# Kernel optimization log

Measured on AMD Instinct MI355X. Metric: run time of the kernel, lower is better.

The kernel has to match this reference:

```python
import jax, jax.numpy as jnp
import numpy as np

NT = 128          # num_timesteps (reference query points)
E = 128           # embed_time
H = 128           # nhidden
NH = 1            # num_heads
F = 32            # feature_size
NS = 2            # num_states
EPS = 1e-5


def layer_norm(x, g, b):
    m = jnp.mean(x, axis=-1, keepdims=True)
    v = jnp.mean((x - m) ** 2, axis=-1, keepdims=True)
    return (x - m) * jax.lax.rsqrt(v + EPS) * g + b


def setup_inputs() -> dict:
    key = jax.random.key(0)
    ks = jax.random.split(key, 24)
    nrm = lambda k, s: (jax.random.normal(k, s) * 0.05).astype(jnp.float32)
    inp = {
        "input": jax.random.normal(ks[0], (8, F, 512), dtype=jnp.float32),
        "mask": jax.random.randint(ks[1], (8, F, 512), 0, 2).astype(jnp.float32),
        "timesteps": jnp.sort(jax.random.uniform(ks[2], (8, 512), dtype=jnp.float32), axis=-1),
        # time embedding
        "periodic_w": nrm(ks[3], (E - 1, 1)), "periodic_b": nrm(ks[4], (E - 1,)),
        "lin_w": nrm(ks[5], (1, 1)), "lin_b": nrm(ks[6], (1,)),
        # query / key projections + layer norms
        "q_w": nrm(ks[7], (E, E)), "q_b": nrm(ks[8], (E,)),
        "q_g": jnp.ones((E,), jnp.float32), "q_be": jnp.zeros((E,), jnp.float32),
        "k_w": nrm(ks[9], (E, E)), "k_b": nrm(ks[10], (E,)),
        "k_g": jnp.ones((E,), jnp.float32), "k_be": jnp.zeros((E,), jnp.float32),
        # attention_norm over h*2F channels, then output linear + LN to nhidden
        "attn_g": jnp.ones((NH * 2 * F,), jnp.float32), "attn_b": jnp.zeros((NH * 2 * F,), jnp.float32),
        "out_w": nrm(ks[11], (H, NH * 2 * F)), "out_b": nrm(ks[12], (H,)),
        "out_g": jnp.ones((H,), jnp.float32), "out_be": jnp.zeros((H,), jnp.float32),
        # GRU (torch gate order r, z, n)
        "gru_wih": nrm(ks[13], (3 * H, H)), "gru_whh": nrm(ks[14], (3 * H, H)),
        "gru_bih": nrm(ks[15], (3 * H,)), "gru_bhh": nrm(ks[16], (3 * H,)),
        # classifier MLP
        "c1_w": nrm(ks[17], (H, H)), "c1_b": nrm(ks[18], (H,)),
        "c2_w": nrm(ks[19], (H, H)), "c2_b": nrm(ks[20], (H,)),
        "c3_w": nrm(ks[21], (NS, H)), "c3_b": nrm(ks[22], (NS,)),
    }
    return inp


def time_embedding(tt, lin_w, lin_b, periodic_w, periodic_b):
    t = tt[..., None]                                   # (..., 1)
    out1 = t @ lin_w.T + lin_b                          # (..., 1)
    out2 = jnp.sin(t @ periodic_w.T + periodic_b)       # (..., E-1)
    return jnp.concatenate([out1, out2], axis=-1)       # (..., E)


def reference(input, mask, timesteps, periodic_w, periodic_b, lin_w, lin_b,
              q_w, q_b, q_g, q_be, k_w, k_b, k_g, k_be,
              attn_g, attn_b, out_w, out_b, out_g, out_be,
              gru_wih, gru_whh, gru_bih, gru_bhh,
              c1_w, c1_b, c2_w, c2_b, c3_w, c3_b):
    B = input.shape[0]
    x_in = jnp.transpose(input, (0, 2, 1))              # (B, T, F)
    m = 1.0 - jnp.transpose(mask, (0, 2, 1))            # (B, T, F)
    x_in = x_in * (m > 0).astype(x_in.dtype)
    x = jnp.concatenate([x_in, m], axis=-1)             # (B, T, 2F)
    mk = jnp.concatenate([m, m], axis=-1)               # (B, T, 2F)

    key_e = time_embedding(timesteps, lin_w, lin_b, periodic_w, periodic_b)        # (B, T, E)
    qtimes = jnp.linspace(0.0, 1.0, NT)
    query_e = time_embedding(qtimes[None], lin_w, lin_b, periodic_w, periodic_b)   # (1, NT, E)

    q = layer_norm(query_e @ q_w.T + q_b, q_g, q_be)    # (1, NT, E)
    k = layer_norm(key_e @ k_w.T + k_b, k_g, k_be)      # (B, T, E)

    etk = E // NH
    q = q.reshape(1, NT, NH, etk).transpose(0, 2, 1, 3)         # (1, h, NT, etk)
    k = k.reshape(B, -1, NH, etk).transpose(0, 2, 1, 3)         # (B, h, T, etk)

    scores = jnp.einsum("ahqd,bhkd->bhqk", q, k) / np.sqrt(etk)  # (B, h, NT, T)
    # per-channel masked softmax over keys: (B, h, NT, T, 2F)
    logits = jnp.where(mk[:, None, None, :, :] == 0, -1e9, scores[..., None])
    p_attn = jax.nn.softmax(logits, axis=-2)
    att = jnp.sum(p_attn * x[:, None, None, :, :], axis=-2)     # (B, h, NT, 2F)

    x2 = att.transpose(0, 2, 1, 3).reshape(B, NT, NH * 2 * F)
    x2 = layer_norm(x2, attn_g, attn_b)
    out = layer_norm(x2 @ out_w.T + out_b, out_g, out_be)       # (B, NT, H)

    # GRU over the NT reference timesteps, last hidden state
    seq = out.transpose(1, 0, 2)                                # (NT, B, H)
    h0 = jnp.zeros((B, H), out.dtype)

    def gru_step(h, x_t):
        gi = x_t @ gru_wih.T + gru_bih
        gh = h @ gru_whh.T + gru_bhh
        ir, iz, inn = jnp.split(gi, 3, axis=-1)
        hr, hz, hn = jnp.split(gh, 3, axis=-1)
        r = jax.nn.sigmoid(ir + hr)
        z = jax.nn.sigmoid(iz + hz)
        n = jnp.tanh(inn + r * hn)
        h_new = (1.0 - z) * n + z * h
        return h_new, None

    h_last, _ = jax.lax.scan(gru_step, h0, seq)

    h1 = jax.nn.relu(h_last @ c1_w.T + c1_b)
    h2 = jax.nn.relu(h1 @ c2_w.T + c2_b)
    return h2 @ c3_w.T + c3_b                                   # (B, num_states) logits
```

## Files before the change

### kernel.cpp

```cpp
#include <hip/hip_runtime.h>
#include <math.h>

#define LN_EPS 1e-5f

typedef _Float16 h2v __attribute__((ext_vector_type(2)));

__device__ __forceinline__ float dot4(float4 a, float4 b) {
    return a.x*b.x + a.y*b.y + a.z*b.z + a.w*b.w;
}
__device__ __forceinline__ void fma4(float4& a, float s, float4 v) {
    a.x += s*v.x; a.y += s*v.y; a.z += s*v.z; a.w += s*v.w;
}
__device__ __forceinline__ float fast_rcp(float x) {
    return __builtin_amdgcn_rcpf(x);
}
__device__ __forceinline__ float fast_sigmoid(float x) {
    return fast_rcp(1.f + __expf(-x));
}
__device__ __forceinline__ float fast_tanh(float x) {
    return 1.f - 2.f*fast_rcp(__expf(2.f*x) + 1.f);
}
__device__ __forceinline__ float fdot2u(unsigned int a, unsigned int b, float c) {
#if __has_builtin(__builtin_amdgcn_fdot2)
    return __builtin_amdgcn_fdot2(__builtin_bit_cast(h2v, a),
                                  __builtin_bit_cast(h2v, b), c, false);
#else
    const h2v av = __builtin_bit_cast(h2v, a);
    const h2v bv = __builtin_bit_cast(h2v, b);
    return c + (float)av[0]*(float)bv[0] + (float)av[1]*(float)bv[1];
#endif
}
__device__ __forceinline__ float wsum64(float v) {
    #pragma unroll
    for (int off = 32; off > 0; off >>= 1) v += __shfl_xor(v, off);
    return v;
}

__global__ void k_embed_proj(
    const float* __restrict__ input, const float* __restrict__ mask,
    const float* __restrict__ timesteps,
    const float* __restrict__ pw, const float* __restrict__ pb,
    const float* __restrict__ lw, const float* __restrict__ lb,
    const float* __restrict__ q_w, const float* __restrict__ q_b,
    const float* __restrict__ q_g, const float* __restrict__ q_be,
    const float* __restrict__ k_w, const float* __restrict__ k_b,
    const float* __restrict__ k_g, const float* __restrict__ k_be,
    float* __restrict__ qs, float* __restrict__ kT, float2* __restrict__ xm)
{
    const int blk = blockIdx.x;
    const int tid = threadIdx.x;

    __shared__ __align__(16) float e[4][128];
    __shared__ __align__(16) float4 red[128];
    __shared__ __align__(16) float proj[4][128];
    __shared__ __align__(16) float2 tile[32][65];

    if (blk < 64) {
        const int b  = blk >> 3;
        const int t0 = (blk & 7) * 64;
        const int cg = tid >> 6;
        const int tt = tid & 63;
        #pragma unroll
        for (int c16 = 0; c16 < 16; ++c16) {
            const int c = c16*2 + cg;
            const float m = mask [(size_t)(b*32 + c)*512 + t0 + tt];
            const float x = input[(size_t)(b*32 + c)*512 + t0 + tt];
            const float mm = 1.0f - m;
            tile[c][tt] = make_float2(x*mm, mm);
        }
        __syncthreads();
        const int c2 = tid & 31;
        const int tg = tid >> 5;
        #pragma unroll
        for (int k = 0; k < 16; ++k) {
            const int t = tg*16 + k;
            xm[((size_t)b*512 + t0 + t)*32 + c2] = tile[c2][t];
        }
        return;
    }

    const bool isq = blk < 96;
    float tv[4];
    int kidx0 = 0;
    if (isq) {
        const int q0 = (blk - 64) * 4;
        #pragma unroll
        for (int r = 0; r < 4; ++r) tv[r] = (float)(q0 + r) * (1.0f/127.0f);
    } else {
        kidx0 = (blk - 96) * 4;
        #pragma unroll
        for (int r = 0; r < 4; ++r) tv[r] = timesteps[kidx0 + r];
    }

    float pwj = 0.f, pbj = 0.f;
    if (tid > 0) { pwj = pw[tid-1]; pbj = pb[tid-1]; }
    const float lw0 = lw[0], lb0 = lb[0];
    #pragma unroll
    for (int r = 0; r < 4; ++r)
        e[r][tid] = (tid == 0) ? (tv[r]*lw0 + lb0) : sinf(tv[r]*pwj + pbj);
    __syncthreads();

    const float* W  = isq ? q_w  : k_w;
    const float* Bv = isq ? q_b  : k_b;
    const float* G  = isq ? q_g  : k_g;
    const float* Be = isq ? q_be : k_be;

    {
        const int jj = tid >> 2, dc = tid & 3;
        const float4* e0 = (const float4*)(&e[0][0]);
        const float4* e1 = (const float4*)(&e[1][0]);
        const float4* e2 = (const float4*)(&e[2][0]);
        const float4* e3 = (const float4*)(&e[3][0]);
        #pragma unroll
        for (int jb = 0; jb < 4; ++jb) {
            const int j = jb*32 + jj;
            const float4* wrow = (const float4*)(W + (size_t)j*128);
            float a0=0.f, a1=0.f, a2=0.f, a3=0.f;
            #pragma unroll
            for (int k = 0; k < 8; ++k) {
                const int idx = dc + 4*k;
                const float4 w4 = wrow[idx];
                a0 += dot4(w4, e0[idx]);
                a1 += dot4(w4, e1[idx]);
                a2 += dot4(w4, e2[idx]);
                a3 += dot4(w4, e3[idx]);
            }
            a0 += __shfl_xor(a0, 1, 4); a0 += __shfl_xor(a0, 2, 4);
            a1 += __shfl_xor(a1, 1, 4); a1 += __shfl_xor(a1, 2, 4);
            a2 += __shfl_xor(a2, 1, 4); a2 += __shfl_xor(a2, 2, 4);
            a3 += __shfl_xor(a3, 1, 4); a3 += __shfl_xor(a3, 2, 4);
            if (dc == 0) {
                const float bj = Bv[j];
                proj[0][j] = a0 + bj; proj[1][j] = a1 + bj;
                proj[2][j] = a2 + bj; proj[3][j] = a3 + bj;
            }
        }
    }
    __syncthreads();

    float acc[4];
    #pragma unroll
    for (int r = 0; r < 4; ++r) acc[r] = proj[r][tid];

    red[tid] = make_float4(acc[0], acc[1], acc[2], acc[3]);
    __syncthreads();
    for (int s = 64; s > 0; s >>= 1) {
        if (tid < s) {
            float4 m = red[tid]; const float4 o = red[tid+s];
            m.x += o.x; m.y += o.y; m.z += o.z; m.w += o.w;
            red[tid] = m;
        }
        __syncthreads();
    }
    float4 mean = red[0];
    mean.x *= (1.0f/128.0f); mean.y *= (1.0f/128.0f);
    mean.z *= (1.0f/128.0f); mean.w *= (1.0f/128.0f);
    __syncthreads();
    const float d0 = acc[0]-mean.x, d1 = acc[1]-mean.y,
                d2 = acc[2]-mean.z, d3 = acc[3]-mean.w;
    red[tid] = make_float4(d0*d0, d1*d1, d2*d2, d3*d3);
    __syncthreads();
    for (int s = 64; s > 0; s >>= 1) {
        if (tid < s) {
            float4 m = red[tid]; const float4 o = red[tid+s];
            m.x += o.x; m.y += o.y; m.z += o.z; m.w += o.w;
            red[tid] = m;
        }
        __syncthreads();
    }
    float4 var = red[0];
    var.x *= (1.0f/128.0f); var.y *= (1.0f/128.0f);
    var.z *= (1.0f/128.0f); var.w *= (1.0f/128.0f);

    const float gg = G[tid], bb = Be[tid];
    const float o0 = d0*rsqrtf(var.x+LN_EPS)*gg + bb;
    const float o1 = d1*rsqrtf(var.y+LN_EPS)*gg + bb;
    const float o2 = d2*rsqrtf(var.z+LN_EPS)*gg + bb;
    const float o3 = d3*rsqrtf(var.w+LN_EPS)*gg + bb;

    if (isq) {
        const float sc = 0.08838834764831845f;
        const int q0 = (blk - 64)*4;
        qs[(size_t)(q0+0)*128 + tid] = o0*sc;
        qs[(size_t)(q0+1)*128 + tid] = o1*sc;
        qs[(size_t)(q0+2)*128 + tid] = o2*sc;
        qs[(size_t)(q0+3)*128 + tid] = o3*sc;
    } else {
        const int b = kidx0 >> 9;
        const int t = kidx0 & 511;
        *(float4*)(kT + ((size_t)(b*128 + tid))*512 + t) =
            make_float4(o0, o1, o2, o3);
    }
}

__global__ void __launch_bounds__(256) k_attn(
    const float2* __restrict__ xm,
    const float* __restrict__ qs, const float* __restrict__ kT,
    const float* __restrict__ attn_g, const float* __restrict__ attn_b,
    const float* __restrict__ out_w, const float* __restrict__ out_b,
    const float* __restrict__ out_g, const float* __restrict__ out_be,
    float* __restrict__ outm)
{
    const int b     = blockIdx.x >> 5;
    const int qbase = (blockIdx.x & 31) * 4;
    const int tid   = threadIdx.x;

    __shared__ __align__(16) float et[4][512];
    __shared__ __align__(16) float qsh[4][128];
    __shared__ __align__(16) float wsh[128*66];
    __shared__ __align__(16) float sA[4][8][32];
    __shared__ __align__(16) float aA[4][8][32];
    __shared__ __align__(16) float x2s[4][64];
    __shared__ float redC[4];

    for (int idx = tid; idx < 512; idx += 256)
        qsh[idx >> 7][idx & 127] = qs[(size_t)(qbase + (idx >> 7))*128 + (idx & 127)];
    for (int idx = tid; idx < 8192; idx += 256)
        wsh[(idx >> 6)*66 + (idx & 63)] = out_w[idx];
    __syncthreads();

    {
        const int grp = tid >> 7;
        const int tl  = tid & 127;
        const int q0  = grp*2;
        const float4* kp  = (const float4*)kT + (size_t)b*128*128 + tl;
        const float4* qa4 = (const float4*)qsh[q0];
        const float4* qb4 = (const float4*)qsh[q0+1];
        float4 a0 = make_float4(0,0,0,0), a1 = make_float4(0,0,0,0);
        float4 c0 = kp[0], c1 = kp[128], c2 = kp[256], c3 = kp[384];
        for (int c = 0; c < 32; ++c) {
            float4 n0, n1, n2, n3;
            if (c < 31) {
                const float4* kn = kp + (size_t)(4*c+4)*128;
                n0 = kn[0]; n1 = kn[128]; n2 = kn[256]; n3 = kn[384];
            }
            const float4 qa = qa4[c], qb = qb4[c];
            fma4(a0, qa.x, c0); fma4(a1, qb.x, c0);
            fma4(a0, qa.y, c1); fma4(a1, qb.y, c1);
            fma4(a0, qa.z, c2); fma4(a1, qb.z, c2);
            fma4(a0, qa.w, c3); fma4(a1, qb.w, c3);
            c0 = n0; c1 = n1; c2 = n2; c3 = n3;
        }
        a0.x = __expf(a0.x); a0.y = __expf(a0.y); a0.z = __expf(a0.z); a0.w = __expf(a0.w);
        a1.x = __expf(a1.x); a1.y = __expf(a1.y); a1.z = __expf(a1.z); a1.w = __expf(a1.w);
        ((float4*)et[q0])[tl]   = a0;
        ((float4*)et[q0+1])[tl] = a1;
    }
    __syncthreads();

    {
        const int c   = tid & 31;
        const int seg = tid >> 5;
        const float2* xp = xm + ((size_t)b*512 + seg*64)*32 + c;
        float s0=0,s1=0,s2=0,s3=0, a0=0,a1=0,a2=0,a3=0;
        #pragma unroll 4
        for (int i = 0; i < 64; ++i) {
            const float2 v = xp[(size_t)i*32];
            const int t = seg*64 + i;
            const float w0 = et[0][t]*v.y, w1 = et[1][t]*v.y;
            const float w2 = et[2][t]*v.y, w3 = et[3][t]*v.y;
            s0 += w0; s1 += w1; s2 += w2; s3 += w3;
            a0 += w0*v.x; a1 += w1*v.x; a2 += w2*v.x; a3 += w3*v.x;
        }
        sA[0][seg][c]=s0; sA[1][seg][c]=s1; sA[2][seg][c]=s2; sA[3][seg][c]=s3;
        aA[0][seg][c]=a0; aA[1][seg][c]=a1; aA[2][seg][c]=a2; aA[3][seg][c]=a3;
    }
    __syncthreads();

    {
        const int ql = tid >> 6;
        const int c2 = tid & 63;
        const int cc = c2 & 31;
        float ss = 0.f;
        #pragma unroll
        for (int g = 0; g < 8; ++g) ss += sA[ql][g][cc];
        float attv;
        if (c2 < 32) {
            float aa = 0.f;
            #pragma unroll
            for (int g = 0; g < 8; ++g) aa += aA[ql][g][cc];
            attv = (ss > 0.f) ? aa/ss : 0.f;
        } else {
            attv = (ss > 0.f) ? 1.0f : 0.0f;
        }
        const float mean = wsum64(attv) * (1.0f/64.0f);
        const float dv = attv - mean;
        const float var = wsum64(dv*dv) * (1.0f/64.0f);
        x2s[ql][c2] = dv*rsqrtf(var+LN_EPS)*attn_g[c2] + attn_b[c2];
    }
    __syncthreads();

    {
        const int jhalf = tid >> 7;
        const int j     = tid & 127;
        const int wave  = tid >> 6;
        for (int lq2 = 0; lq2 < 2; ++lq2) {
            const int ql = jhalf*2 + lq2;
            float acc = out_b[j];
            const float4* wrow = (const float4*)(wsh + j*66);
            const float4* xr   = (const float4*)x2s[ql];
            #pragma unroll
            for (int k = 0; k < 16; ++k) acc += dot4(wrow[k], xr[k]);

            float v = wsum64(acc);
            if ((tid & 63) == 0) redC[wave] = v;
            __syncthreads();
            const float mean = (redC[jhalf*2] + redC[jhalf*2+1]) * (1.0f/128.0f);
            __syncthreads();
            const float d = acc - mean;
            v = wsum64(d*d);
            if ((tid & 63) == 0) redC[wave] = v;
            __syncthreads();
            const float var = (redC[jhalf*2] + redC[jhalf*2+1]) * (1.0f/128.0f);
            outm[((size_t)b*128 + qbase + ql)*128 + j] =
                d*rsqrtf(var+LN_EPS)*out_g[j] + out_be[j];
            __syncthreads();
        }
    }
}

__global__ void k_gi(const float* __restrict__ outm,
                     const float* __restrict__ wih, const float* __restrict__ bih,
                     float* __restrict__ gi)
{
    const int qi  = blockIdx.x;
    const int tid = threadIdx.x;
    __shared__ __align__(16) float rows[8][128];
    for (int idx = tid; idx < 1024; idx += 384) {
        const int b = idx >> 7, d = idx & 127;
        rows[b][d] = outm[(size_t)(b*128+qi)*128 + d];
    }
    __syncthreads();

    const int g0 = tid >> 2, dc = tid & 3;
    #pragma unroll
    for (int gb = 0; gb < 4; ++gb) {
        const int g = gb*96 + g0;
        const float4* wrow = (const float4*)(wih + (size_t)g*128);
        float acc[8] = {0,0,0,0,0,0,0,0};
        #pragma unroll
        for (int k = 0; k < 8; ++k) {
            const int idx = dc + 4*k;
            const float4 w4 = wrow[idx];
            #pragma unroll
            for (int b = 0; b < 8; ++b)
                acc[b] += dot4(w4, ((const float4*)rows[b])[idx]);
        }
        #pragma unroll
        for (int b = 0; b < 8; ++b) {
            acc[b] += __shfl_xor(acc[b], 1, 4);
            acc[b] += __shfl_xor(acc[b], 2, 4);
        }
        if (dc == 0) {
            const float bi = bih[g];
            #pragma unroll
            for (int b = 0; b < 8; ++b)
                gi[((size_t)qi*8 + b)*384 + g] = acc[b] + bi;
        }
    }
}

__global__ void __launch_bounds__(512) k_gru_cls(
    const float* __restrict__ gi,
    const float* __restrict__ whh, const float* __restrict__ bhh,
    const float* __restrict__ c1w, const float* __restrict__ c1b,
    const float* __restrict__ c2w, const float* __restrict__ c2b,
    const float* __restrict__ c3w, const float* __restrict__ c3b,
    float* __restrict__ out)
{
    const int b   = blockIdx.x;
    const int tid = threadIdx.x;
    const int s   = tid >> 7;
    const int u   = tid & 127;

    __shared__ __align__(16) unsigned int lds[25344];
    unsigned int* hP = lds;
    float4* part4 = (float4*)&lds[64];
    float* hcls = (float*)&lds[64 + 1536];

    {
        const float4* w4 = (const float4*)whh;
        #pragma unroll 4
        for (int k = 0; k < 24; ++k) {
            const int idx = tid + k*512;
            const float4 v = w4[idx];
            const int row = idx >> 5, c4 = idx & 31;
            h2v p0; p0[0] = (_Float16)v.x; p0[1] = (_Float16)v.y;
            h2v p1; p1[0] = (_Float16)v.z; p1[1] = (_Float16)v.w;
            lds[row*66 + c4*2    ] = __builtin_bit_cast(unsigned int, p0);
            lds[row*66 + c4*2 + 1] = __builtin_bit_cast(unsigned int, p1);
        }
    }
    __syncthreads();

    unsigned int wreg[3][16];
    #pragma unroll
    for (int g = 0; g < 3; ++g) {
        const uint2* src = (const uint2*)&lds[(g*128 + u)*66 + 16*s];
        #pragma unroll
        for (int i = 0; i < 8; ++i) {
            const uint2 t = src[i];
            wreg[g][2*i] = t.x; wreg[g][2*i+1] = t.y;
        }
    }
    __syncthreads();

    const float* gbase = gi + (size_t)b*384;
    float bh_r=0.f, bh_z=0.f, bh_n=0.f, gr0=0.f, gz0=0.f, gn0=0.f, hprev=0.f;
    if (tid < 64) hP[tid] = 0u;
    if (s == 0) {
        bh_r = bhh[u]; bh_z = bhh[u+128]; bh_n = bhh[u+256];
        gr0 = gbase[u]; gz0 = gbase[u+128]; gn0 = gbase[u+256];
    }
    __syncthreads();

    for (int qi = 0; qi < 128; ++qi) {
        const uint4* hp4 = (const uint4*)hP + s*4;
        float ar = 0.f, az = 0.f, an = 0.f;
        #pragma unroll
        for (int i = 0; i < 4; ++i) {
            const uint4 hv = hp4[i];
            ar = fdot2u(wreg[0][4*i+0], hv.x, ar);
            ar = fdot2u(wreg[0][4*i+1], hv.y, ar);
            ar = fdot2u(wreg[0][4*i+2], hv.z, ar);
            ar = fdot2u(wreg[0][4*i+3], hv.w, ar);
            az = fdot2u(wreg[1][4*i+0], hv.x, az);
            az = fdot2u(wreg[1][4*i+1], hv.y, az);
            az = fdot2u(wreg[1][4*i+2], hv.z, az);
            az = fdot2u(wreg[1][4*i+3], hv.w, az);
            an = fdot2u(wreg[2][4*i+0], hv.x, an);
            an = fdot2u(wreg[2][4*i+1], hv.y, an);
            an = fdot2u(wreg[2][4*i+2], hv.z, an);
            an = fdot2u(wreg[2][4*i+3], hv.w, an);
        }
        if (s > 0) part4[(s-1)*128 + u] = make_float4(ar, az, an, 0.f);

        float grn=0.f, gzn=0.f, gnn=0.f;
        if (s == 0 && qi < 127) {
            const float* gb = gbase + (size_t)(qi+1)*3072;
            grn = gb[u]; gzn = gb[u+128]; gnn = gb[u+256];
        }
        __syncthreads();

        if (s == 0) {
            const float4 p0 = part4[u], p1 = part4[128+u], p2 = part4[256+u];
            const float ghr = ar + p0.x + p1.x + p2.x + bh_r;
            const float ghz = az + p0.y + p1.y + p2.y + bh_z;
            const float ghn = an + p0.z + p1.z + p2.z + bh_n;
            const float r = fast_sigmoid(gr0 + ghr);
            const float z = fast_sigmoid(gz0 + ghz);
            const float n = fast_tanh(gn0 + r*ghn);
            const float hn2 = (1.f - z)*n + z*hprev;
            hprev = hn2;
            gr0 = grn; gz0 = gzn; gn0 = gnn;
            const float other = __shfl_xor(hn2, 1);
            if ((u & 1) == 0) {
                h2v hp; hp[0] = (_Float16)hn2; hp[1] = (_Float16)other;
                hP[u >> 1] = __builtin_bit_cast(unsigned int, hp);
            }
        }
        __syncthreads();
    }

    float* scr = (float*)part4;
    if (s == 0) hcls[u] = hprev;
    __syncthreads();
    if (tid < 128) {
        float acc = c1b[u];
        const float4* wc = (const float4*)(c1w + (size_t)u*128);
        const float4* v  = (const float4*)hcls;
        #pragma unroll
        for (int d4 = 0; d4 < 32; ++d4) acc += dot4(wc[d4], v[d4]);
        scr[u] = fmaxf(acc, 0.f);
    }
    __syncthreads();
    if (tid < 128) {
        float acc = c2b[u];
        const float4* wc = (const float4*)(c2w + (size_t)u*128);
        const float4* v  = (const float4*)scr;
        #pragma unroll
        for (int d4 = 0; d4 < 32; ++d4) acc += dot4(wc[d4], v[d4]);
        scr[128 + u] = fmaxf(acc, 0.f);
    }
    __syncthreads();
    if (tid < 2) {
        float acc = c3b[tid];
        const float4* wc = (const float4*)(c3w + (size_t)tid*128);
        const float4* v  = (const float4*)(scr + 128);
        #pragma unroll
        for (int d4 = 0; d4 < 32; ++d4) acc += dot4(wc[d4], v[d4]);
        out[(size_t)b*2 + tid] = acc;
    }
}

extern "C" void kernel_launch(void* const* d_in, const int* in_sizes, int n_in,
                              void* d_out, int out_size, void* d_ws, size_t ws_size,
                              hipStream_t stream)
{
    const float* input     = (const float*)d_in[0];
    const float* mask      = (const float*)d_in[1];
    const float* timesteps = (const float*)d_in[2];
    const float* pw        = (const float*)d_in[3];
    const float* pb        = (const float*)d_in[4];
    const float* lw        = (const float*)d_in[5];
    const float* lb        = (const float*)d_in[6];
    const float* q_w       = (const float*)d_in[7];
    const float* q_b       = (const float*)d_in[8];
    const float* q_g       = (const float*)d_in[9];
    const float* q_be      = (const float*)d_in[10];
    const float* k_w       = (const float*)d_in[11];
    const float* k_b       = (const float*)d_in[12];
    const float* k_g       = (const float*)d_in[13];
    const float* k_be      = (const float*)d_in[14];
    const float* attn_g    = (const float*)d_in[15];
    const float* attn_b    = (const float*)d_in[16];
    const float* out_w     = (const float*)d_in[17];
    const float* out_b     = (const float*)d_in[18];
    const float* out_g     = (const float*)d_in[19];
    const float* out_be    = (const float*)d_in[20];
    const float* gru_wih   = (const float*)d_in[21];
    const float* gru_whh   = (const float*)d_in[22];
    const float* gru_bih   = (const float*)d_in[23];
    const float* gru_bhh   = (const float*)d_in[24];
    const float* c1_w      = (const float*)d_in[25];
    const float* c1_b      = (const float*)d_in[26];
    const float* c2_w      = (const float*)d_in[27];
    const float* c2_b      = (const float*)d_in[28];
    const float* c3_w      = (const float*)d_in[29];
    const float* c3_b      = (const float*)d_in[30];

    float* ws   = (float*)d_ws;
    float*  qs   = ws;
    float*  kT   = qs   + 16384;
    float*  outm = kT   + 524288;
    float*  gi   = outm + 131072;
    float2* xm   = (float2*)(gi + 393216);

    k_embed_proj<<<1120, 128, 0, stream>>>(input, mask, timesteps,
                                           pw, pb, lw, lb,
                                           q_w, q_b, q_g, q_be,
                                           k_w, k_b, k_g, k_be, qs, kT, xm);
    k_attn<<<256, 256, 0, stream>>>(xm, qs, kT,
                                    attn_g, attn_b, out_w, out_b,
                                    out_g, out_be, outm);
    k_gi<<<128, 384, 0, stream>>>(outm, gru_wih, gru_bih, gi);
    k_gru_cls<<<8, 512, 0, stream>>>(gi, gru_whh, gru_bhh,
                                     c1_w, c1_b, c2_w, c2_b, c3_w, c3_b,
                                     (float*)d_out);
}
```

Before: 238.1 us.

## Restructure GRU recurrence: lane-quad K split with DPP reduction, double-buffered hidden state

```diff
diff --git a/kernel.cpp b/kernel.cpp
--- a/kernel.cpp
+++ b/kernel.cpp
@@ -34,6 +34,16 @@
     #pragma unroll
     for (int off = 32; off > 0; off >>= 1) v += __shfl_xor(v, off);
     return v;
+}
+__device__ __forceinline__ float qadd_xor1(float v) {
+    const int x = __builtin_amdgcn_mov_dpp(__builtin_bit_cast(int, v),
+                                           0xB1 , 0xF, 0xF, true);
+    return v + __builtin_bit_cast(float, x);
+}
+__device__ __forceinline__ float qadd_xor2(float v) {
+    const int x = __builtin_amdgcn_mov_dpp(__builtin_bit_cast(int, v),
+                                           0x4E , 0xF, 0xF, true);
+    return v + __builtin_bit_cast(float, x);
 }
 
 __global__ void k_embed_proj(
@@ -370,117 +380,109 @@
 {
     const int b   = blockIdx.x;
     const int tid = threadIdx.x;
-    const int s   = tid >> 7;
-    const int u   = tid & 127;
-
-    __shared__ __align__(16) unsigned int lds[25344];
-    unsigned int* hP = lds;
-    float4* part4 = (float4*)&lds[64];
-    float* hcls = (float*)&lds[64 + 1536];
-
-    {
-        const float4* w4 = (const float4*)whh;
-        #pragma unroll 4
-        for (int k = 0; k < 24; ++k) {
-            const int idx = tid + k*512;
-            const float4 v = w4[idx];
-            const int row = idx >> 5, c4 = idx & 31;
-            h2v p0; p0[0] = (_Float16)v.x; p0[1] = (_Float16)v.y;
-            h2v p1; p1[0] = (_Float16)v.z; p1[1] = (_Float16)v.w;
-            lds[row*66 + c4*2    ] = __builtin_bit_cast(unsigned int, p0);
-            lds[row*66 + c4*2 + 1] = __builtin_bit_cast(unsigned int, p1);
-        }
-    }
-    __syncthreads();
+    const int u   = tid >> 2;
+    const int s   = tid & 3;
+
+    __shared__ __align__(16) unsigned int hbuf[2][64];
+    __shared__ __align__(16) float hcls[128];
+    __shared__ __align__(16) float scr[256];
 
     unsigned int wreg[3][16];
     #pragma unroll
     for (int g = 0; g < 3; ++g) {
-        const uint2* src = (const uint2*)&lds[(g*128 + u)*66 + 16*s];
+        const float4* wrow = (const float4*)(whh + (size_t)(g*128 + u)*128 + 32*s);
         #pragma unroll
         for (int i = 0; i < 8; ++i) {
-            const uint2 t = src[i];
-            wreg[g][2*i] = t.x; wreg[g][2*i+1] = t.y;
-        }
-    }
-    __syncthreads();
+            const float4 v = wrow[i];
+            h2v p0; p0[0] = (_Float16)v.x; p0[1] = (_Float16)v.y;
+            h2v p1; p1[0] = (_Float16)v.z; p1[1] = (_Float16)v.w;
+            wreg[g][2*i]   = __builtin_bit_cast(unsigned int, p0);
+            wreg[g][2*i+1] = __builtin_bit_cast(unsigned int, p1);
+        }
+    }
+    const float bh_r = bhh[u], bh_z = bhh[u+128], bh_n = bhh[u+256];
 
     const float* gbase = gi + (size_t)b*384;
-    float bh_r=0.f, bh_z=0.f, bh_n=0.f, gr0=0.f, gz0=0.f, gn0=0.f, hprev=0.f;
-    if (tid < 64) hP[tid] = 0u;
-    if (s == 0) {
-        bh_r = bhh[u]; bh_z = bhh[u+128]; bh_n = bhh[u+256];
-        gr0 = gbase[u]; gz0 = gbase[u+128]; gn0 = gbase[u+256];
-    }
-    __syncthreads();
-
-    for (int qi = 0; qi < 128; ++qi) {
-        const uint4* hp4 = (const uint4*)hP + s*4;
-        float ar = 0.f, az = 0.f, an = 0.f;
-        #pragma unroll
-        for (int i = 0; i < 4; ++i) {
-            const uint4 hv = hp4[i];
-            ar = fdot2u(wreg[0][4*i+0], hv.x, ar);
-            ar = fdot2u(wreg[0][4*i+1], hv.y, ar);
-            ar = fdot2u(wreg[0][4*i+2], hv.z, ar);
-            ar = fdot2u(wreg[0][4*i+3], hv.w, ar);
-            az = fdot2u(wreg[1][4*i+0], hv.x, az);
-            az = fdot2u(wreg[1][4*i+1], hv.y, az);
-            az = fdot2u(wreg[1][4*i+2], hv.z, az);
-            az = fdot2u(wreg[1][4*i+3], hv.w, az);
-            an = fdot2u(wreg[2][4*i+0], hv.x, an);
-            an = fdot2u(wreg[2][4*i+1], hv.y, an);
-            an = fdot2u(wreg[2][4*i+2], hv.z, an);
-            an = fdot2u(wreg[2][4*i+3], hv.w, an);
-        }
-        if (s > 0) part4[(s-1)*128 + u] = make_float4(ar, az, an, 0.f);
-
-        float grn=0.f, gzn=0.f, gnn=0.f;
-        if (s == 0 && qi < 127) {
-            const float* gb = gbase + (size_t)(qi+1)*3072;
-            grn = gb[u]; gzn = gb[u+128]; gnn = gb[u+256];
-        }
+    float gR0 = gbase[u],        gZ0 = gbase[u+128],        gN0 = gbase[u+256];
+    float gR1 = gbase[3072+u],   gZ1 = gbase[3072+u+128],   gN1 = gbase[3072+u+256];
+
+    if (tid < 128) ((unsigned int*)hbuf)[tid] = 0u;
+    float hprev = 0.f;
+    __syncthreads();
+
+#define GRU_STEP(RB, WB, GR, GZ, GN, PF)                                       \
+    {                                                                          \
+        const uint4* hp4 = (const uint4*)hbuf[RB] + s*4;                       \
+        uint4 hv[4];                                                           \
+        hv[0] = hp4[0]; hv[1] = hp4[1]; hv[2] = hp4[2]; hv[3] = hp4[3];        \
+        const float* gb = gbase + (size_t)(PF)*3072;                           \
+        const float tR = gb[u], tZ = gb[u+128], tN = gb[u+256];                \
+        float ar[2] = {0.f,0.f}, az[2] = {0.f,0.f}, an[2] = {0.f,0.f};         \
+        _Pragma("unroll")                                                      \
+        for (int i = 0; i < 4; ++i) {                                          \
+            const int p = i >> 1;                                              \
+            ar[p] = fdot2u(wreg[0][4*i+0], hv[i].x, ar[p]);                    \
+            ar[p] = fdot2u(wreg[0][4*i+1], hv[i].y, ar[p]);                    \
+            ar[p] = fdot2u(wreg[0][4*i+2], hv[i].z, ar[p]);                    \
+            ar[p] = fdot2u(wreg[0][4*i+3], hv[i].w, ar[p]);                    \
+            az[p] = fdot2u(wreg[1][4*i+0], hv[i].x, az[p]);                    \
+            az[p] = fdot2u(wreg[1][4*i+1], hv[i].y, az[p]);                    \
+            az[p] = fdot2u(wreg[1][4*i+2], hv[i].z, az[p]);                    \
+            az[p] = fdot2u(wreg[1][4*i+3], hv[i].w, az[p]);                    \
+            an[p] = fdot2u(wreg[2][4*i+0], hv[i].x, an[p]);                    \
+            an[p] = fdot2u(wreg[2][4*i+1], hv[i].y, an[p]);                    \
+            an[p] = fdot2u(wreg[2][4*i+2], hv[i].z, an[p]);                    \
+            an[p] = fdot2u(wreg[2][4*i+3], hv[i].w, an[p]);                    \
+        }                                                                      \
+        float arr = ar[0] + ar[1];                                             \
+        float azz = az[0] + az[1];                                             \
+        float ann = an[0] + an[1];                                             \
+        arr = qadd_xor1(arr); arr = qadd_xor2(arr);                            \
+        azz = qadd_xor1(azz); azz = qadd_xor2(azz);                            \
+        ann = qadd_xor1(ann); ann = qadd_xor2(ann);                            \
+        const float ghr = arr + bh_r;                                          \
+        const float ghz = azz + bh_z;                                          \
+        const float ghn = ann + bh_n;                                          \
+        const float r = fast_sigmoid(GR + ghr);                                \
+        const float z = fast_sigmoid(GZ + ghz);                                \
+        const float n = fast_tanh(GN + r*ghn);                                 \
+        const float hn2 = (1.f - z)*n + z*hprev;                               \
+        hprev = hn2;                                                           \
+        GR = tR; GZ = tZ; GN = tN;                                             \
+        const float other = __shfl_xor(hn2, 4);                               \
+        if ((tid & 7) == 0) {                                                  \
+            h2v hp; hp[0] = (_Float16)hn2; hp[1] = (_Float16)other;            \
+            hbuf[WB][tid >> 3] = __builtin_bit_cast(unsigned int, hp);         \
+        }                                                                      \
+    }
+
+    #pragma unroll 1
+    for (int qi = 0; qi < 128; qi += 2) {
+        GRU_STEP(0, 1, gR0, gZ0, gN0, (qi+2 < 128 ? qi+2 : 127));
         __syncthreads();
-
-        if (s == 0) {
-            const float4 p0 = part4[u], p1 = part4[128+u], p2 = part4[256+u];
-            const float ghr = ar + p0.x + p1.x + p2.x + bh_r;
-            const float ghz = az + p0.y + p1.y + p2.y + bh_z;
-            const float ghn = an + p0.z + p1.z + p2.z + bh_n;
-            const float r = fast_sigmoid(gr0 + ghr);
-            const float z = fast_sigmoid(gz0 + ghz);
-            const float n = fast_tanh(gn0 + r*ghn);
-            const float hn2 = (1.f - z)*n + z*hprev;
-            hprev = hn2;
-            gr0 = grn; gz0 = gzn; gn0 = gnn;
-            const float other = __shfl_xor(hn2, 1);
-            if ((u & 1) == 0) {
-                h2v hp; hp[0] = (_Float16)hn2; hp[1] = (_Float16)other;
-                hP[u >> 1] = __builtin_bit_cast(unsigned int, hp);
-            }
-        }
+        GRU_STEP(1, 0, gR1, gZ1, gN1, (qi+3 < 128 ? qi+3 : 127));
         __syncthreads();
     }
-
-    float* scr = (float*)part4;
-    if (s == 0) hcls[u] = hprev;
+#undef GRU_STEP
+
+    if ((tid & 3) == 0) hcls[u] = hprev;
     __syncthreads();
     if (tid < 128) {
-        float acc = c1b[u];
-        const float4* wc = (const float4*)(c1w + (size_t)u*128);
+        float acc = c1b[tid];
+        const float4* wc = (const float4*)(c1w + (size_t)tid*128);
         const float4* v  = (const float4*)hcls;
         #pragma unroll
         for (int d4 = 0; d4 < 32; ++d4) acc += dot4(wc[d4], v[d4]);
-        scr[u] = fmaxf(acc, 0.f);
+        scr[tid] = fmaxf(acc, 0.f);
     }
     __syncthreads();
     if (tid < 128) {
-        float acc = c2b[u];
-        const float4* wc = (const float4*)(c2w + (size_t)u*128);
+        float acc = c2b[tid];
+        const float4* wc = (const float4*)(c2w + (size_t)tid*128);
         const float4* v  = (const float4*)scr;
         #pragma unroll
         for (int d4 = 0; d4 < 32; ++d4) acc += dot4(wc[d4], v[d4]);
-        scr[128 + u] = fmaxf(acc, 0.f);
+        scr[128 + tid] = fmaxf(acc, 0.f);
     }
     __syncthreads();
     if (tid < 2) {
```

Measured after the change: 229.5 us. 3.6% less time.
